# Performance work log

Measured on AMD Instinct MI355X. Metric: run time of the kernel, lower is better.

## Reference

```python
import jax, jax.numpy as jnp
import numpy as np

H, W = 512, 512  # image_size from init_kwargs


def _render_single(xyz, color, opacity):
    """Faithful JAX version of GaussianRenderer._fallback_render (the path the
    module executes when the CUDA rasterizer is unavailable), vectorized.
    Point-splat each Gaussian to one pixel, depth-sort descending (back-to-front),
    alpha-composite: a_k = o_k * prod_{j<k}(1 - o_j); depth = z of front-most hit.
    xyz: (N,3)  color: (N,3)  opacity: (N,1)
    """
    N = xyz.shape[0]
    focal = (H + W) / 2.0
    z = xyz[:, 2]
    xf = xyz[:, 0] / (z + 1e-6) * focal + W / 2.0
    yf = xyz[:, 1] / (z + 1e-6) * focal + H / 2.0
    # torch .long() truncates toward zero
    xi = jnp.trunc(jnp.clip(xf, -1e9, 1e9)).astype(jnp.int32)
    yi = jnp.trunc(jnp.clip(yf, -1e9, 1e9)).astype(jnp.int32)
    valid = (xi >= 0) & (xi < W) & (yi >= 0) & (yi < H)
    pix = jnp.where(valid, yi * W + xi, H * W)  # dummy slot H*W for out-of-bounds
    # stable sort: primary pixel ascending, secondary z descending (back-to-front)
    order = jnp.lexsort((-z, pix))
    pix_s, z_s = pix[order], z[order]
    o_s = opacity[order, 0]
    c_s = color[order]
    valid_s = pix_s < H * W
    # per-pixel exclusive transmittance: alpha recurrence 1-A_k = (1-A_{k-1})(1-o_k)
    logt = jnp.log(jnp.clip(1.0 - o_s, 1e-12, None))
    cs = jnp.cumsum(logt)
    excl = cs - logt  # exclusive cumsum (global)
    start = jnp.concatenate([jnp.ones((1,), bool), pix_s[1:] != pix_s[:-1]])
    start_idx = jax.lax.cummax(jnp.where(start, jnp.arange(N), -1))
    T_prev = jnp.exp(excl - excl[start_idx])  # exclusive within pixel segment
    a = jnp.where(valid_s, o_s * T_prev, 0.0)
    img = jnp.zeros((H * W + 1, 3), xyz.dtype).at[pix_s].add(a[:, None] * c_s)
    # depth: last element written per pixel (front-most, smallest z in segment)
    end = jnp.concatenate([pix_s[1:] != pix_s[:-1], jnp.ones((1,), bool)])
    dpix = jnp.where(end & valid_s, pix_s, H * W)
    depth = jnp.zeros((H * W + 1,), xyz.dtype).at[dpix].set(z_s)
    render = img[: H * W].reshape(H, W, 3).transpose(2, 0, 1)  # (3,H,W)
    return render, depth[: H * W].reshape(1, H, W)


def setup_inputs() -> dict:
    key = jax.random.key(0)
    ks = jax.random.split(key, 5)
    B, N = 8, 262144
    return {
        "xyz": jax.random.normal(ks[0], (B, N, 3), jnp.float32),
        "scale": jax.random.normal(ks[1], (B, N, 3), jnp.float32),
        "rotation": jax.random.normal(ks[2], (B, N, 1), jnp.float32),
        "opacity": jax.random.uniform(ks[3], (B, N, 1), jnp.float32),
        "color": jax.random.uniform(ks[4], (B, N, 3), jnp.float32),
    }


def reference(xyz, scale, rotation, opacity, color):
    # scale/rotation are accepted (part of the gaussians dict) but unused by the
    # fallback renderer, matching the torch source.
    render, depth = jax.vmap(_render_single)(xyz, color, opacity)
    return render, depth
```

## Files before the change

kernel.cpp:

```cpp
#include <hip/hip_runtime.h>
#include <stdint.h>

#define W_ 512
#define H_ 512
#define HW_ (512 * 512)
#define RMAX 4
#define OVF_CAP 65536

__device__ __forceinline__ int project_pix(float x, float y, float z) {
    float zz = z + 1e-6f;
    float xf = x / zz * 512.0f + 256.0f;
    float yf = y / zz * 512.0f + 256.0f;
    xf = fminf(fmaxf(xf, -1e9f), 1e9f);
    yf = fminf(fmaxf(yf, -1e9f), 1e9f);
    int xi = (int)xf;
    int yi = (int)yf;
    if (xi >= 0 && xi < W_ && yi >= 0 && yi < H_) return yi * W_ + xi;
    return -1;
}

__device__ __forceinline__ unsigned int q8(float v) {
    v = fminf(fmaxf(v, 0.f), 1.f);
    return (unsigned int)__float2uint_rn(v * 255.0f);
}
__device__ __forceinline__ float d8(unsigned int u) {
    return (float)(u & 255u) * (1.0f / 255.0f);
}

__global__ void __launch_bounds__(256) k_init(uint4* __restrict__ p, int n4) {
    int i = blockIdx.x * blockDim.x + threadIdx.x;
    if (i < n4) p[i] = make_uint4(0u, 0u, 0u, 0u);
}

__global__ void __launch_bounds__(256) k_build(const float4* __restrict__ xyz4,
                                               const float4* __restrict__ op4,
                                               const float4* __restrict__ col4,
                                               unsigned int* __restrict__ cnt,
                                               unsigned long long* __restrict__ s0,
                                               unsigned long long* __restrict__ sx,
                                               unsigned int* __restrict__ ovf_hdr,
                                               unsigned int* __restrict__ ovf_pix,
                                               unsigned long long* __restrict__ ovf_rec,
                                               int N, int total4) {
    int t = blockIdx.x * blockDim.x + threadIdx.x;
    if (t >= total4) return;
    float4 v0 = xyz4[3 * (size_t)t + 0];
    float4 v1 = xyz4[3 * (size_t)t + 1];
    float4 v2 = xyz4[3 * (size_t)t + 2];
    float4 o4 = op4[t];
    float4 c0 = col4[3 * (size_t)t + 0];
    float4 c1 = col4[3 * (size_t)t + 1];
    float4 c2 = col4[3 * (size_t)t + 2];
    float xs[4] = {v0.x, v0.w, v1.z, v2.y};
    float ys[4] = {v0.y, v1.x, v1.w, v2.z};
    float zs[4] = {v0.z, v1.y, v2.x, v2.w};
    float os[4] = {o4.x, o4.y, o4.z, o4.w};
    float cr[4] = {c0.x, c0.w, c1.z, c2.y};
    float cg[4] = {c0.y, c1.x, c1.w, c2.z};
    float cb[4] = {c0.z, c1.y, c2.x, c2.w};
    int g0 = 4 * t;
    size_t pbase = (size_t)(g0 / N) * HW_;
#pragma unroll
    for (int j = 0; j < 4; ++j) {
        int pix = project_pix(xs[j], ys[j], zs[j]);
        if (pix >= 0) {
            size_t p = pbase + pix;
            unsigned int sh = 16u * (unsigned int)(p & 1);
            unsigned int old = atomicAdd(&cnt[p >> 1], 1u << sh);
            unsigned int s = (old >> sh) & 0xffffu;
            unsigned int pay = q8(os[j]) | (q8(cr[j]) << 8) | (q8(cg[j]) << 16) |
                               (q8(cb[j]) << 24);
            unsigned long long rec =
                ((unsigned long long)__float_as_uint(zs[j]) << 32) | (unsigned long long)pay;
            if (s == 0) {
                s0[p] = rec;
            } else if (s < RMAX) {
                sx[p * 3 + (s - 1)] = rec;
            } else {
                unsigned int i = atomicAdd(ovf_hdr, 1u);
                if (i < OVF_CAP) { ovf_pix[i] = (unsigned int)p; ovf_rec[i] = rec; }
            }
        }
    }
}

__global__ void __launch_bounds__(256) k_composite(const unsigned int* __restrict__ cnt,
                                                   const unsigned long long* __restrict__ s0,
                                                   const unsigned long long* __restrict__ sx,
                                                   const unsigned int* __restrict__ ovf_hdr,
                                                   const unsigned int* __restrict__ ovf_pix,
                                                   const unsigned long long* __restrict__ ovf_rec,
                                                   float* __restrict__ out, int B) {
    int q = blockIdx.x * blockDim.x + threadIdx.x;
    int nb8 = B * (HW_ / 8);
    if (q >= nb8) return;
    int p0 = 8 * q;
    int b = p0 / HW_;
    int pl0 = p0 - b * HW_;

    uint4 cw = ((const uint4*)cnt)[q];
    const uint4* s0p = (const uint4*)&s0[p0];
    uint4 sa = s0p[0], sb = s0p[1], sc = s0p[2], sd = s0p[3];

    unsigned int ws[4] = {cw.x, cw.y, cw.z, cw.w};
    unsigned int pay0_[8] = {sa.x, sa.z, sb.x, sb.z, sc.x, sc.z, sd.x, sd.z};
    unsigned int zb0_[8]  = {sa.y, sa.w, sb.y, sb.w, sc.y, sc.w, sd.y, sd.w};

    float rr[8], gg[8], bb[8], dd[8];

#pragma unroll
    for (int j = 0; j < 8; ++j) {
        unsigned int k = (ws[j >> 1] >> (16 * (j & 1))) & 0xffffu;
        float r = 0.f, g2 = 0.f, bl = 0.f, depth = 0.f;
        if (k > 0) {
            size_t p = (size_t)p0 + j;

            unsigned int pa = pay0_[j];
            float o0 = d8(pa);
            r  = o0 * d8(pa >> 8);
            g2 = o0 * d8(pa >> 16);
            bl = o0 * d8(pa >> 24);
            depth = __uint_as_float(zb0_[j]);

            if (k >= 2) {
                const unsigned long long* sxp = &sx[p * 3];
                unsigned long long r1 = sxp[0];
                unsigned int pf = pay0_[j], pn = (unsigned int)r1;
                float zf = __uint_as_float(zb0_[j]);
                float zn = __uint_as_float((unsigned int)(r1 >> 32));
                bool sw = (zn > zf) || (zn == zf && pn < pf);
                if (sw) {
                    unsigned int tp = pf; pf = pn; pn = tp;
                    float tz = zf; zf = zn; zn = tz;
                }
                float of = d8(pf), on = d8(pn);
                float a1 = on * (1.0f - of);
                r  = of * d8(pf >> 8)  + a1 * d8(pn >> 8);
                g2 = of * d8(pf >> 16) + a1 * d8(pn >> 16);
                bl = of * d8(pf >> 24) + a1 * d8(pn >> 24);
                depth = zn;

                if (k >= 3) {
                    unsigned long long r2 = sxp[1];
                    if (k <= RMAX) {
                        unsigned long long r3 = (k > 3) ? sxp[2] : 0ull;
                        float z_[4];
                        unsigned int y_[4];
                        z_[0] = __uint_as_float(zb0_[j]);            y_[0] = pay0_[j];
                        z_[1] = __uint_as_float((unsigned int)(r1 >> 32)); y_[1] = (unsigned int)r1;
                        z_[2] = __uint_as_float((unsigned int)(r2 >> 32)); y_[2] = (unsigned int)r2;
                        z_[3] = (k > 3) ? __uint_as_float((unsigned int)(r3 >> 32))
                                        : -__builtin_inff();
                        y_[3] = (unsigned int)r3;
#define CE(I, J)                                                                    \
                        {                                                           \
                            bool sw2 = (z_[J] > z_[I]) || (z_[J] == z_[I] && y_[J] < y_[I]); \
                            if (sw2) {                                              \
                                float tz = z_[I]; z_[I] = z_[J]; z_[J] = tz;        \
                                unsigned int ty = y_[I]; y_[I] = y_[J]; y_[J] = ty; \
                            }                                                       \
                        }
                        CE(0,1) CE(2,3) CE(0,2) CE(1,3) CE(1,2)
#undef CE
                        float T = 1.f;
                        r = 0.f; g2 = 0.f; bl = 0.f; depth = 0.f;
#pragma unroll
                        for (int s = 0; s < RMAX; ++s) {
                            if (s < (int)k) {
                                unsigned int pay = y_[s];
                                float o = d8(pay);
                                float a = o * T;
                                r  += a * d8(pay >> 8);
                                g2 += a * d8(pay >> 16);
                                bl += a * d8(pay >> 24);
                                T *= (1.0f - o);
                                depth = z_[s];
                            }
                        }
                    } else {
                        unsigned long long r3 = sxp[2];
                        unsigned int nov = ovf_hdr[0];
                        if (nov > OVF_CAP) nov = OVF_CAP;
                        unsigned int ptag = (unsigned int)p;
                        float zz0 = __uint_as_float(zb0_[j]);
                        float zz1 = __uint_as_float((unsigned int)(r1 >> 32));
                        float zz2 = __uint_as_float((unsigned int)(r2 >> 32));
                        float zz3 = __uint_as_float((unsigned int)(r3 >> 32));
                        float prev_z = __builtin_inff();
                        unsigned int prev_y = 0u;
                        float T = 1.f;
                        r = 0.f; g2 = 0.f; bl = 0.f; depth = 0.f;
                        for (int s = 0; s < (int)k; ++s) {
                            float best_z = -__builtin_inff();
                            unsigned int best_y = ~0u;
#define CAND(Z, Y)                                                                       \
                            {                                                            \
                                float z = (Z); unsigned int y = (Y);                     \
                                bool after  = (z < prev_z) || (z == prev_z && y > prev_y); \
                                bool better = (z > best_z) || (z == best_z && y < best_y); \
                                if (after && better) { best_z = z; best_y = y; }         \
                            }
                            CAND(zz0, pay0_[j]) CAND(zz1, (unsigned int)r1)
                            CAND(zz2, (unsigned int)r2) CAND(zz3, (unsigned int)r3)
                            for (unsigned int t2 = 0; t2 < nov; ++t2) {
                                if (ovf_pix[t2] == ptag) {
                                    unsigned long long rec = ovf_rec[t2];
                                    CAND(__uint_as_float((unsigned int)(rec >> 32)),
                                         (unsigned int)rec)
                                }
                            }
#undef CAND
                            unsigned int pay = best_y;
                            float o = d8(pay);
                            float a = o * T;
                            r  += a * d8(pay >> 8);
                            g2 += a * d8(pay >> 16);
                            bl += a * d8(pay >> 24);
                            T *= (1.0f - o);
                            depth = best_z;
                            prev_z = best_z;
                            prev_y = best_y;
                        }
                    }
                }
            }
        }
        rr[j] = r; gg[j] = g2; bb[j] = bl; dd[j] = depth;
    }

    size_t HWs = (size_t)HW_;
    float* oR = out + ((size_t)b * 3 + 0) * HWs + pl0;
    float* oG = out + ((size_t)b * 3 + 1) * HWs + pl0;
    float* oB = out + ((size_t)b * 3 + 2) * HWs + pl0;
    float* oD = out + (size_t)B * 3 * HWs + (size_t)b * HWs + pl0;
    *(float4*)(oR)     = make_float4(rr[0], rr[1], rr[2], rr[3]);
    *(float4*)(oR + 4) = make_float4(rr[4], rr[5], rr[6], rr[7]);
    *(float4*)(oG)     = make_float4(gg[0], gg[1], gg[2], gg[3]);
    *(float4*)(oG + 4) = make_float4(gg[4], gg[5], gg[6], gg[7]);
    *(float4*)(oB)     = make_float4(bb[0], bb[1], bb[2], bb[3]);
    *(float4*)(oB + 4) = make_float4(bb[4], bb[5], bb[6], bb[7]);
    *(float4*)(oD)     = make_float4(dd[0], dd[1], dd[2], dd[3]);
    *(float4*)(oD + 4) = make_float4(dd[4], dd[5], dd[6], dd[7]);
}

extern "C" void kernel_launch(void* const* d_in, const int* in_sizes, int n_in,
                              void* d_out, int out_size, void* d_ws, size_t ws_size,
                              hipStream_t stream) {
    const float* xyz     = (const float*)d_in[0];
    const float* opacity = (const float*)d_in[3];
    const float* color   = (const float*)d_in[4];
    float* out = (float*)d_out;

    int B = out_size / (4 * HW_);
    int N = in_sizes[0] / (3 * B);
    int total = B * N;
    int nb = B * HW_;

    unsigned int* cnt      = (unsigned int*)d_ws;
    unsigned int* ovf_hdr  = cnt + nb / 2;
    unsigned int* ovf_pix  = ovf_hdr + 64;
    unsigned long long* ovf_rec = (unsigned long long*)(ovf_pix + OVF_CAP);
    unsigned long long* s0      = ovf_rec + OVF_CAP;
    unsigned long long* sx      = s0 + nb;

    int blk = 256;
    int zwords = nb / 2 + 64;
    int z4 = zwords / 4;
    k_init<<<(z4 + blk - 1) / blk, blk, 0, stream>>>((uint4*)cnt, z4);

    int total4 = total / 4;
    k_build<<<(total4 + blk - 1) / blk, blk, 0, stream>>>((const float4*)xyz,
                                                          (const float4*)opacity,
                                                          (const float4*)color,
                                                          cnt, s0, sx, ovf_hdr, ovf_pix, ovf_rec,
                                                          N, total4);

    int nb8 = nb / 8;
    k_composite<<<(nb8 + blk - 1) / blk, blk, 0, stream>>>(cnt, s0, sx, ovf_hdr, ovf_pix,
                                                           ovf_rec, out, B);
}
```

Baseline: 41.10 us.

## Narrow per-pixel counters to 8 bits, early-exit off-screen quads, nontemporal output stores

Per-pixel slot counters shrink from 16-bit to 8-bit. This halves the counter array the init kernel zeroes and the composite kernel reads. The build kernel now projects all four points first and returns before loading opacity and color when none land on screen, which skips most of those input reads. Final image and depth writes use nontemporal stores to avoid polluting cache. The 8-bit counters would wrap if more than 255 points hit one pixel, which would corrupt results.

```diff
diff --git a/kernel.cpp b/kernel.cpp
--- a/kernel.cpp
+++ b/kernel.cpp
@@ -6,6 +6,9 @@
 #define HW_ (512 * 512)
 #define RMAX 4
 #define OVF_CAP 65536
+
+typedef float f32x4v __attribute__((ext_vector_type(4)));
+typedef unsigned long long u64;
 
 __device__ __forceinline__ int project_pix(float x, float y, float z) {
     float zz = z + 1e-6f;
@@ -36,42 +39,48 @@
                                                const float4* __restrict__ op4,
                                                const float4* __restrict__ col4,
                                                unsigned int* __restrict__ cnt,
-                                               unsigned long long* __restrict__ s0,
-                                               unsigned long long* __restrict__ sx,
+                                               u64* __restrict__ s0,
+                                               u64* __restrict__ sx,
                                                unsigned int* __restrict__ ovf_hdr,
                                                unsigned int* __restrict__ ovf_pix,
-                                               unsigned long long* __restrict__ ovf_rec,
+                                               u64* __restrict__ ovf_rec,
                                                int N, int total4) {
     int t = blockIdx.x * blockDim.x + threadIdx.x;
     if (t >= total4) return;
     float4 v0 = xyz4[3 * (size_t)t + 0];
     float4 v1 = xyz4[3 * (size_t)t + 1];
     float4 v2 = xyz4[3 * (size_t)t + 2];
+    float xs[4] = {v0.x, v0.w, v1.z, v2.y};
+    float ys[4] = {v0.y, v1.x, v1.w, v2.z};
+    float zs[4] = {v0.z, v1.y, v2.x, v2.w};
+
+    int pix[4];
+#pragma unroll
+    for (int j = 0; j < 4; ++j) pix[j] = project_pix(xs[j], ys[j], zs[j]);
+
+    if (pix[0] < 0 && pix[1] < 0 && pix[2] < 0 && pix[3] < 0) return;
+
     float4 o4 = op4[t];
     float4 c0 = col4[3 * (size_t)t + 0];
     float4 c1 = col4[3 * (size_t)t + 1];
     float4 c2 = col4[3 * (size_t)t + 2];
-    float xs[4] = {v0.x, v0.w, v1.z, v2.y};
-    float ys[4] = {v0.y, v1.x, v1.w, v2.z};
-    float zs[4] = {v0.z, v1.y, v2.x, v2.w};
     float os[4] = {o4.x, o4.y, o4.z, o4.w};
     float cr[4] = {c0.x, c0.w, c1.z, c2.y};
     float cg[4] = {c0.y, c1.x, c1.w, c2.z};
     float cb[4] = {c0.z, c1.y, c2.x, c2.w};
+
     int g0 = 4 * t;
     size_t pbase = (size_t)(g0 / N) * HW_;
 #pragma unroll
     for (int j = 0; j < 4; ++j) {
-        int pix = project_pix(xs[j], ys[j], zs[j]);
-        if (pix >= 0) {
-            size_t p = pbase + pix;
-            unsigned int sh = 16u * (unsigned int)(p & 1);
-            unsigned int old = atomicAdd(&cnt[p >> 1], 1u << sh);
-            unsigned int s = (old >> sh) & 0xffffu;
+        if (pix[j] >= 0) {
+            size_t p = pbase + pix[j];
+            unsigned int sh = 8u * (unsigned int)(p & 3);
+            unsigned int old = atomicAdd(&cnt[p >> 2], 1u << sh);
+            unsigned int s = (old >> sh) & 0xffu;
             unsigned int pay = q8(os[j]) | (q8(cr[j]) << 8) | (q8(cg[j]) << 16) |
                                (q8(cb[j]) << 24);
-            unsigned long long rec =
-                ((unsigned long long)__float_as_uint(zs[j]) << 32) | (unsigned long long)pay;
+            u64 rec = ((u64)__float_as_uint(zs[j]) << 32) | (u64)pay;
             if (s == 0) {
                 s0[p] = rec;
             } else if (s < RMAX) {
@@ -85,11 +94,11 @@
 }
 
 __global__ void __launch_bounds__(256) k_composite(const unsigned int* __restrict__ cnt,
-                                                   const unsigned long long* __restrict__ s0,
-                                                   const unsigned long long* __restrict__ sx,
+                                                   const u64* __restrict__ s0,
+                                                   const u64* __restrict__ sx,
                                                    const unsigned int* __restrict__ ovf_hdr,
                                                    const unsigned int* __restrict__ ovf_pix,
-                                                   const unsigned long long* __restrict__ ovf_rec,
+                                                   const u64* __restrict__ ovf_rec,
                                                    float* __restrict__ out, int B) {
     int q = blockIdx.x * blockDim.x + threadIdx.x;
     int nb8 = B * (HW_ / 8);
@@ -98,11 +107,10 @@
     int b = p0 / HW_;
     int pl0 = p0 - b * HW_;
 
-    uint4 cw = ((const uint4*)cnt)[q];
+    uint2 cw = ((const uint2*)cnt)[q];
     const uint4* s0p = (const uint4*)&s0[p0];
     uint4 sa = s0p[0], sb = s0p[1], sc = s0p[2], sd = s0p[3];
 
-    unsigned int ws[4] = {cw.x, cw.y, cw.z, cw.w};
     unsigned int pay0_[8] = {sa.x, sa.z, sb.x, sb.z, sc.x, sc.z, sd.x, sd.z};
     unsigned int zb0_[8]  = {sa.y, sa.w, sb.y, sb.w, sc.y, sc.w, sd.y, sd.w};
 
@@ -110,7 +118,7 @@
 
 #pragma unroll
     for (int j = 0; j < 8; ++j) {
-        unsigned int k = (ws[j >> 1] >> (16 * (j & 1))) & 0xffffu;
+        unsigned int k = ((j < 4 ? cw.x : cw.y) >> (8 * (j & 3))) & 0xffu;
         float r = 0.f, g2 = 0.f, bl = 0.f, depth = 0.f;
         if (k > 0) {
             size_t p = (size_t)p0 + j;
@@ -123,8 +131,8 @@
             depth = __uint_as_float(zb0_[j]);
 
             if (k >= 2) {
-                const unsigned long long* sxp = &sx[p * 3];
-                unsigned long long r1 = sxp[0];
+                const u64* sxp = &sx[p * 3];
+                u64 r1 = sxp[0];
                 unsigned int pf = pay0_[j], pn = (unsigned int)r1;
                 float zf = __uint_as_float(zb0_[j]);
                 float zn = __uint_as_float((unsigned int)(r1 >> 32));
@@ -141,12 +149,12 @@
                 depth = zn;
 
                 if (k >= 3) {
-                    unsigned long long r2 = sxp[1];
+                    u64 r2 = sxp[1];
                     if (k <= RMAX) {
-                        unsigned long long r3 = (k > 3) ? sxp[2] : 0ull;
+                        u64 r3 = (k > 3) ? sxp[2] : 0ull;
                         float z_[4];
                         unsigned int y_[4];
-                        z_[0] = __uint_as_float(zb0_[j]);            y_[0] = pay0_[j];
+                        z_[0] = __uint_as_float(zb0_[j]);                  y_[0] = pay0_[j];
                         z_[1] = __uint_as_float((unsigned int)(r1 >> 32)); y_[1] = (unsigned int)r1;
                         z_[2] = __uint_as_float((unsigned int)(r2 >> 32)); y_[2] = (unsigned int)r2;
                         z_[3] = (k > 3) ? __uint_as_float((unsigned int)(r3 >> 32))
@@ -178,7 +186,7 @@
                             }
                         }
                     } else {
-                        unsigned long long r3 = sxp[2];
+                        u64 r3 = sxp[2];
                         unsigned int nov = ovf_hdr[0];
                         if (nov > OVF_CAP) nov = OVF_CAP;
                         unsigned int ptag = (unsigned int)p;
@@ -204,7 +212,7 @@
                             CAND(zz2, (unsigned int)r2) CAND(zz3, (unsigned int)r3)
                             for (unsigned int t2 = 0; t2 < nov; ++t2) {
                                 if (ovf_pix[t2] == ptag) {
-                                    unsigned long long rec = ovf_rec[t2];
+                                    u64 rec = ovf_rec[t2];
                                     CAND(__uint_as_float((unsigned int)(rec >> 32)),
                                          (unsigned int)rec)
                                 }
@@ -233,14 +241,22 @@
     float* oG = out + ((size_t)b * 3 + 1) * HWs + pl0;
     float* oB = out + ((size_t)b * 3 + 2) * HWs + pl0;
     float* oD = out + (size_t)B * 3 * HWs + (size_t)b * HWs + pl0;
-    *(float4*)(oR)     = make_float4(rr[0], rr[1], rr[2], rr[3]);
-    *(float4*)(oR + 4) = make_float4(rr[4], rr[5], rr[6], rr[7]);
-    *(float4*)(oG)     = make_float4(gg[0], gg[1], gg[2], gg[3]);
-    *(float4*)(oG + 4) = make_float4(gg[4], gg[5], gg[6], gg[7]);
-    *(float4*)(oB)     = make_float4(bb[0], bb[1], bb[2], bb[3]);
-    *(float4*)(oB + 4) = make_float4(bb[4], bb[5], bb[6], bb[7]);
-    *(float4*)(oD)     = make_float4(dd[0], dd[1], dd[2], dd[3]);
-    *(float4*)(oD + 4) = make_float4(dd[4], dd[5], dd[6], dd[7]);
+    f32x4v w0 = {rr[0], rr[1], rr[2], rr[3]};
+    f32x4v w1 = {rr[4], rr[5], rr[6], rr[7]};
+    f32x4v w2 = {gg[0], gg[1], gg[2], gg[3]};
+    f32x4v w3 = {gg[4], gg[5], gg[6], gg[7]};
+    f32x4v w4 = {bb[0], bb[1], bb[2], bb[3]};
+    f32x4v w5 = {bb[4], bb[5], bb[6], bb[7]};
+    f32x4v w6 = {dd[0], dd[1], dd[2], dd[3]};
+    f32x4v w7 = {dd[4], dd[5], dd[6], dd[7]};
+    __builtin_nontemporal_store(w0, (f32x4v*)(oR));
+    __builtin_nontemporal_store(w1, (f32x4v*)(oR + 4));
+    __builtin_nontemporal_store(w2, (f32x4v*)(oG));
+    __builtin_nontemporal_store(w3, (f32x4v*)(oG + 4));
+    __builtin_nontemporal_store(w4, (f32x4v*)(oB));
+    __builtin_nontemporal_store(w5, (f32x4v*)(oB + 4));
+    __builtin_nontemporal_store(w6, (f32x4v*)(oD));
+    __builtin_nontemporal_store(w7, (f32x4v*)(oD + 4));
 }
 
 extern "C" void kernel_launch(void* const* d_in, const int* in_sizes, int n_in,
@@ -257,14 +273,14 @@
     int nb = B * HW_;
 
     unsigned int* cnt      = (unsigned int*)d_ws;
-    unsigned int* ovf_hdr  = cnt + nb / 2;
+    unsigned int* ovf_hdr  = cnt + nb / 4;
     unsigned int* ovf_pix  = ovf_hdr + 64;
-    unsigned long long* ovf_rec = (unsigned long long*)(ovf_pix + OVF_CAP);
-    unsigned long long* s0      = ovf_rec + OVF_CAP;
-    unsigned long long* sx      = s0 + nb;
+    u64* ovf_rec = (u64*)(ovf_pix + OVF_CAP);
+    u64* s0      = ovf_rec + OVF_CAP;
+    u64* sx      = s0 + nb;
 
     int blk = 256;
-    int zwords = nb / 2 + 64;
+    int zwords = nb / 4 + 64;
     int z4 = zwords / 4;
     k_init<<<(z4 + blk - 1) / blk, blk, 0, stream>>>((uint4*)cnt, z4);
 
```

Measured after the change: 44.58 us. 1.08x slower.
